# Kernel tuning notes

Hardware: AMD Instinct MI355X
Metric: run time of the kernel (lower is better)

## Reference

```python
import jax, jax.numpy as jnp
import numpy as np

N_ENT = 100000
N_REL = 200
D_IN = 128
D_HID = 128
D_OUT = 128
N_BASES = 50
N_EDGES = 800000
N_TRIPLES = 4096
BN_EPS = 1e-5


def setup_inputs() -> dict:
    key = jax.random.key(0)
    ks = jax.random.split(key, 16)
    xavier = lambda k, shape: jax.random.normal(k, shape, jnp.float32) * np.sqrt(2.0 / (shape[-2] + shape[-1]))
    inp = {
        'entity_embeds': xavier(ks[0], (N_ENT, D_IN)),
        'bases': xavier(ks[1], (N_BASES, D_IN)),
        'coefficients': xavier(ks[2], (N_REL, N_BASES)),
        'self_rel_embed': xavier(ks[3], (1, D_IN)),
        'W1': xavier(ks[4], (3, D_IN, D_HID)),
        'relw1': xavier(ks[5], (D_IN, D_HID)),
        'bn1_gamma': jnp.ones((D_HID,), jnp.float32),
        'bn1_beta': jnp.zeros((D_HID,), jnp.float32),
        'W2': xavier(ks[6], (3, D_HID, D_OUT)),
        'relw2': xavier(ks[7], (D_HID, D_OUT)),
        'bn2_gamma': jnp.ones((D_OUT,), jnp.float32),
        'bn2_beta': jnp.zeros((D_OUT,), jnp.float32),
        'ent_ids': jnp.arange(N_ENT, dtype=jnp.int32),
        'edge_index': jax.random.randint(ks[8], (2, N_EDGES), 0, N_ENT, jnp.int32),
        'edge_type': jax.random.randint(ks[9], (N_EDGES,), 0, 2 * N_REL + 1, jnp.int32),
        'y': jax.random.randint(ks[10], (N_EDGES,), 0, 3, jnp.int32),
    }
    heads = jax.random.randint(ks[11], (N_TRIPLES,), 0, N_ENT, jnp.int32)
    rels = jax.random.randint(ks[12], (N_TRIPLES,), 0, 2 * N_REL + 1, jnp.int32)
    tails = jax.random.randint(ks[13], (N_TRIPLES,), 0, N_ENT, jnp.int32)
    inp['triples'] = jnp.stack([heads, rels, tails], axis=1)
    return inp


def _compgcn_layer(x, r, edge_index, edge_type, y, W, relw, gamma, beta):
    src, dst = edge_index[0], edge_index[1]
    # message: gather neighbor & relation embeds, edge-direction-conditioned matmul
    msgs = x[src] - r[edge_type]                      # [E, d_in]
    out = jnp.zeros((msgs.shape[0], W.shape[-1]), msgs.dtype)
    for k in range(3):  # y in {0,1,2}: masked matmul instead of [E,d,d] gather
        mask = (y == k)[:, None]
        out = out + jnp.where(mask, msgs, 0.0) @ W[k]
    # scatter-add aggregation at destination nodes
    agg = jax.ops.segment_sum(out, dst, num_segments=x.shape[0])  # [N, d_out]
    # BatchNorm1d (training-mode batch statistics, biased var)
    mean = jnp.mean(agg, axis=0)
    var = jnp.mean(jnp.square(agg - mean), axis=0)
    bn = (agg - mean) * jax.lax.rsqrt(var + BN_EPS) * gamma + beta
    return jnp.tanh(bn), r @ relw


def reference(entity_embeds, bases, coefficients, self_rel_embed, W1, relw1,
              bn1_gamma, bn1_beta, W2, relw2, bn2_gamma, bn2_beta,
              ent_ids, edge_index, edge_type, y, triples):
    x = entity_embeds[ent_ids]
    r = coefficients @ bases                           # basis-composed relations
    r = jnp.concatenate([r, -r, self_rel_embed], axis=0)  # [2R+1, d]
    x, r = _compgcn_layer(x, r, edge_index, edge_type, y, W1, relw1, bn1_gamma, bn1_beta)
    x, r = _compgcn_layer(x, r, edge_index, edge_type, y, W2, relw2, bn2_gamma, bn2_beta)
    # decode: TransE-style L1 score
    h = x[triples[:, 0]]
    re = r[triples[:, 1]]
    t = x[triples[:, 2]]
    scores = jnp.sum(jnp.abs(h + re - t), axis=1)      # p=1 norm
    return scores
```

## Files before the change

kernel.cpp:

```cpp
#include <hip/hip_runtime.h>
#include <cstdint>

typedef __attribute__((ext_vector_type(8))) short short8;
typedef __attribute__((ext_vector_type(4))) float f32x4;

static __device__ __forceinline__ unsigned short f2bf(float f) {
  unsigned int u = __float_as_uint(f);
  unsigned int r = (u + 0x7FFFu + ((u >> 16) & 1u)) >> 16;
  return (unsigned short)r;
}
static __device__ __forceinline__ unsigned int pack2bf(float a, float b) {
  return (unsigned int)f2bf(a) | ((unsigned int)f2bf(b) << 16);
}
static __device__ __forceinline__ float2 bf2f(unsigned int u) {
  return make_float2(__uint_as_float(u << 16), __uint_as_float(u & 0xFFFF0000u));
}
static __device__ __forceinline__ void acc8(float* a, uint4 h, uint4 r) {
  float2 f, g;
  f = bf2f(h.x); g = bf2f(r.x); a[0] += f.x - g.x; a[1] += f.y - g.y;
  f = bf2f(h.y); g = bf2f(r.y); a[2] += f.x - g.x; a[3] += f.y - g.y;
  f = bf2f(h.z); g = bf2f(r.z); a[4] += f.x - g.x; a[5] += f.y - g.y;
  f = bf2f(h.w); g = bf2f(r.w); a[6] += f.x - g.x; a[7] += f.y - g.y;
}

__global__ void k_rfull(const float* __restrict__ coeff, const float* __restrict__ bases,
                        const float* __restrict__ selfr, float* __restrict__ rfull,
                        unsigned int* __restrict__ rfb) {
  __shared__ float row_s[128];
  int row = blockIdx.x, c = threadIdx.x;
  float v;
  if (row == 400) {
    v = selfr[c];
  } else {
    int rr = row < 200 ? row : row - 200;
    float s = 0.f;
#pragma unroll 10
    for (int b = 0; b < 50; ++b) s += coeff[rr * 50 + b] * bases[b * 128 + c];
    v = (row < 200) ? s : -s;
  }
  rfull[row * 128 + c] = v;
  row_s[c] = v;
  __syncthreads();
  if (c < 64) rfb[row * 64 + c] = pack2bf(row_s[2 * c], row_s[2 * c + 1]);
}

__global__ void k_rmm(const float* __restrict__ A, const float* __restrict__ B,
                      float* __restrict__ out, unsigned int* __restrict__ outb) {
  __shared__ float row_s[128];
  int r = blockIdx.x, c = threadIdx.x;
  float s = 0.f;
#pragma unroll 8
  for (int k = 0; k < 128; ++k) s += A[r * 128 + k] * B[k * 128 + c];
  out[r * 128 + c] = s;
  if (outb) {
    row_s[c] = s;
    __syncthreads();
    if (c < 64) outb[r * 64 + c] = pack2bf(row_s[2 * c], row_s[2 * c + 1]);
  }
}

__global__ void k_cvt(const float* __restrict__ src, unsigned int* __restrict__ dst, int nPairs) {
  int i = blockIdx.x * blockDim.x + threadIdx.x;
  if (i >= nPairs) return;
  float2 v = *(const float2*)&src[(size_t)i * 2];
  dst[i] = pack2bf(v.x, v.y);
}

__global__ void k_wconv2(const float* __restrict__ W1, const float* __restrict__ W2,
                         unsigned short* __restrict__ WT1, unsigned short* __restrict__ WT2) {
  int gid = blockIdx.x * 256 + threadIdx.x;
  const int half = 128 * 384;
  const float* W = (gid < half) ? W1 : W2;
  unsigned short* WT = (gid < half) ? WT1 : WT2;
  int idx = (gid < half) ? gid : gid - half;
  int n = idx & 127, k = idx >> 7;
  int kk = k >> 7, kr = k & 127;
  WT[(size_t)n * 384 + k] = f2bf(W[(size_t)kk * 16384 + kr * 128 + n]);
}

__global__ __launch_bounds__(256) void k_histR(const int* __restrict__ ei, const int* __restrict__ y,
                                               int* __restrict__ counts, int nE, int rsz) {
  int r = blockIdx.x;
  int e0 = blockIdx.y * 1024;
#pragma unroll
  for (int i = 0; i < 4; ++i) {
    int e = e0 + i * 256 + threadIdx.x;
    if (e < nE) {
      int key = ei[nE + e] * 3 + y[e];
      if (key / rsz == r) atomicAdd(&counts[key], 1);
    }
  }
}

__global__ void k_scan1(const int* __restrict__ counts, int* __restrict__ local,
                        int* __restrict__ blockSums, int n) {
  __shared__ int sdata[1024];
  int tid = threadIdx.x;
  int i = blockIdx.x * 1024 + tid;
  int v = (i < n) ? counts[i] : 0;
  sdata[tid] = v;
  __syncthreads();
  for (int off = 1; off < 1024; off <<= 1) {
    int t = (tid >= off) ? sdata[tid - off] : 0;
    __syncthreads();
    sdata[tid] += t;
    __syncthreads();
  }
  if (i < n) local[i] = sdata[tid] - v;
  if (tid == 1023) blockSums[blockIdx.x] = sdata[1023];
}

__global__ void k_scan2(const int* __restrict__ blockSums, int* __restrict__ carries,
                        int* __restrict__ offsets, int n, int nb) {
  __shared__ int sdata[1024];
  int tid = threadIdx.x;
  int v = (tid < nb) ? blockSums[tid] : 0;
  sdata[tid] = v;
  __syncthreads();
  for (int off = 1; off < 1024; off <<= 1) {
    int t = (tid >= off) ? sdata[tid - off] : 0;
    __syncthreads();
    sdata[tid] += t;
    __syncthreads();
  }
  if (tid < nb) carries[tid] = sdata[tid] - v;
  if (tid == 1023) offsets[n] = sdata[1023];
}

__global__ void k_scan3(const int* __restrict__ local, const int* __restrict__ carries,
                        int* __restrict__ offsets, int* __restrict__ cursor, int n) {
  int i = blockIdx.x * 1024 + threadIdx.x;
  if (i >= n) return;
  int v = local[i] + carries[blockIdx.x];
  offsets[i] = v;
  cursor[i] = v;
}

__global__ __launch_bounds__(256) void k_fillR(const int* __restrict__ ei, const int* __restrict__ et,
                                               const int* __restrict__ y, int* __restrict__ cursor,
                                               unsigned int* __restrict__ bucket, int nE, int rsz) {
  int r = blockIdx.x;
  int e0 = blockIdx.y * 1024;
#pragma unroll
  for (int i = 0; i < 4; ++i) {
    int e = e0 + i * 256 + threadIdx.x;
    if (e < nE) {
      int key = ei[nE + e] * 3 + y[e];
      if (key / rsz == r) {
        int slot = atomicAdd(&cursor[key], 1);
        bucket[slot] = (unsigned int)ei[e] | ((unsigned int)et[e] << 20);
      }
    }
  }
}

__global__ __launch_bounds__(256) void k_agg4(const unsigned int* __restrict__ xb,
                                              const int* __restrict__ ids,
                                              const unsigned int* __restrict__ rb,
                                              const int* __restrict__ offsets,
                                              const unsigned int* __restrict__ packed,
                                              unsigned short* __restrict__ T,
                                              float* __restrict__ statZero, int nKeys) {
  if (blockIdx.x == 0) statZero[threadIdx.x] = 0.f;
  int wid = blockIdx.x * 4 + (threadIdx.x >> 6);
  int lane = threadIdx.x & 63;
  int quad = lane >> 4, l16 = lane & 15;
  int key = wid * 4 + quad;
  if (key >= nKeys) return;
  int dst = key / 3, k = key - dst * 3;
  int s = offsets[key], e = offsets[key + 1];
  float a0[8] = {}, a1[8] = {};
  int j = s;
  for (; j + 1 < e; j += 2) {
    unsigned int p0 = packed[j], p1 = packed[j + 1];
    int s0 = p0 & 0xFFFFF, t0 = p0 >> 20;
    int s1 = p1 & 0xFFFFF, t1 = p1 >> 20;
    if (ids) { s0 = ids[s0]; s1 = ids[s1]; }
    uint4 h0 = *(const uint4*)&xb[(size_t)s0 * 64 + l16 * 4];
    uint4 r0 = *(const uint4*)&rb[(size_t)t0 * 64 + l16 * 4];
    uint4 h1 = *(const uint4*)&xb[(size_t)s1 * 64 + l16 * 4];
    uint4 r1 = *(const uint4*)&rb[(size_t)t1 * 64 + l16 * 4];
    acc8(a0, h0, r0);
    acc8(a1, h1, r1);
  }
  if (j < e) {
    unsigned int p0 = packed[j];
    int s0 = p0 & 0xFFFFF, t0 = p0 >> 20;
    if (ids) s0 = ids[s0];
    uint4 h0 = *(const uint4*)&xb[(size_t)s0 * 64 + l16 * 4];
    uint4 r0 = *(const uint4*)&rb[(size_t)t0 * 64 + l16 * 4];
    acc8(a0, h0, r0);
  }
  uint4 o;
  o.x = pack2bf(a0[0] + a1[0], a0[1] + a1[1]);
  o.y = pack2bf(a0[2] + a1[2], a0[3] + a1[3]);
  o.z = pack2bf(a0[4] + a1[4], a0[5] + a1[5]);
  o.w = pack2bf(a0[6] + a1[6], a0[7] + a1[7]);
  *(uint4*)&T[(size_t)dst * 384 + k * 128 + l16 * 8] = o;
}

__global__ __launch_bounds__(256) void k_gemm_mfma(const unsigned short* __restrict__ A,
                                                   const unsigned short* __restrict__ WT,
                                                   unsigned short* __restrict__ C,
                                                   float* __restrict__ sums,
                                                   float* __restrict__ sumsq, int M) {
  __shared__ unsigned short As[2][128][40];
  __shared__ unsigned short Bs[2][128][40];
  __shared__ float sSum[128], sSq[128];
  const int tid = threadIdx.x;
  const int m0 = blockIdx.x * 128;
  const int wave = tid >> 6, lane = tid & 63;
  const int wrow = wave >> 1, wcol = wave & 1;
  const int quad = lane >> 4, l16 = lane & 15;
  f32x4 acc[4][4] = {};

  const int rr0 = tid >> 2, kc0 = (tid & 3) * 8;
  const int rr1 = rr0 + 64;
  const int ma0 = m0 + rr0, ma1 = m0 + rr1;
  const float4 fz = make_float4(0.f, 0.f, 0.f, 0.f);

  float4 apf0, apf1, bpf0, bpf1;
  apf0 = (ma0 < M) ? *(const float4*)&A[(size_t)ma0 * 384 + kc0] : fz;
  apf1 = (ma1 < M) ? *(const float4*)&A[(size_t)ma1 * 384 + kc0] : fz;
  bpf0 = *(const float4*)&WT[(size_t)rr0 * 384 + kc0];
  bpf1 = *(const float4*)&WT[(size_t)rr1 * 384 + kc0];
  *(float4*)&As[0][rr0][kc0] = apf0;
  *(float4*)&As[0][rr1][kc0] = apf1;
  *(float4*)&Bs[0][rr0][kc0] = bpf0;
  *(float4*)&Bs[0][rr1][kc0] = bpf1;
  __syncthreads();

  for (int it = 0; it < 12; ++it) {
    const int cur = it & 1;
    const int nxt = cur ^ 1;
    const bool pf = (it < 11);
    if (pf) {
      int kb = (it + 1) * 32;
      apf0 = (ma0 < M) ? *(const float4*)&A[(size_t)ma0 * 384 + kb + kc0] : fz;
      apf1 = (ma1 < M) ? *(const float4*)&A[(size_t)ma1 * 384 + kb + kc0] : fz;
      bpf0 = *(const float4*)&WT[(size_t)rr0 * 384 + kb + kc0];
      bpf1 = *(const float4*)&WT[(size_t)rr1 * 384 + kb + kc0];
    }
    short8 a[4], b[4];
#pragma unroll
    for (int t = 0; t < 4; ++t) a[t] = *(const short8*)&As[cur][wrow * 64 + t * 16 + l16][quad * 8];
#pragma unroll
    for (int t = 0; t < 4; ++t) b[t] = *(const short8*)&Bs[cur][wcol * 64 + t * 16 + l16][quad * 8];
#pragma unroll
    for (int rt = 0; rt < 4; ++rt)
#pragma unroll
      for (int ct = 0; ct < 4; ++ct)
        acc[rt][ct] = __builtin_amdgcn_mfma_f32_16x16x32_bf16(a[rt], b[ct], acc[rt][ct], 0, 0, 0);
    if (pf) {
      *(float4*)&As[nxt][rr0][kc0] = apf0;
      *(float4*)&As[nxt][rr1][kc0] = apf1;
      *(float4*)&Bs[nxt][rr0][kc0] = bpf0;
      *(float4*)&Bs[nxt][rr1][kc0] = bpf1;
      __syncthreads();
    }
  }

  if (tid < 128) { sSum[tid] = 0.f; sSq[tid] = 0.f; }
  __syncthreads();
  float ps[4] = {}, pq[4] = {};
#pragma unroll
  for (int rt = 0; rt < 4; ++rt) {
#pragma unroll
    for (int reg = 0; reg < 4; ++reg) {
      int m = m0 + wrow * 64 + rt * 16 + quad * 4 + reg;
      if (m < M) {
#pragma unroll
        for (int ct = 0; ct < 4; ++ct) {
          float v = acc[rt][ct][reg];
          int col = wcol * 64 + ct * 16 + l16;
          C[(size_t)m * 128 + col] = f2bf(v);
          ps[ct] += v; pq[ct] += v * v;
        }
      }
    }
  }
#pragma unroll
  for (int ct = 0; ct < 4; ++ct) {
    int col = wcol * 64 + ct * 16 + l16;
    atomicAdd(&sSum[col], ps[ct]);
    atomicAdd(&sSq[col], pq[ct]);
  }
  __syncthreads();
  if (tid < 128) {
    atomicAdd(&sums[tid], sSum[tid]);
    atomicAdd(&sumsq[tid], sSq[tid]);
  }
}

__global__ void k_norm(const unsigned int* __restrict__ Cb,
                       const float* __restrict__ sums, const float* __restrict__ sumsq,
                       const float* __restrict__ gamma, const float* __restrict__ beta,
                       float invN, unsigned int* __restrict__ xb, int nPairs) {
  __shared__ float sc_s[128], bi_s[128];
  if (threadIdx.x < 128) {
    int c = threadIdx.x;
    float mean = sums[c] * invN;
    float var = fmaxf(sumsq[c] * invN - mean * mean, 0.f);
    float sc = rsqrtf(var + 1e-5f) * gamma[c];
    sc_s[c] = sc;
    bi_s[c] = beta[c] - mean * sc;
  }
  __syncthreads();
  int i = blockIdx.x * blockDim.x + threadIdx.x;
  if (i >= nPairs) return;
  int j = i & 63;
  float2 v = bf2f(Cb[i]);
  float a = tanhf(fmaf(v.x, sc_s[2 * j], bi_s[2 * j]));
  float b = tanhf(fmaf(v.y, sc_s[2 * j + 1], bi_s[2 * j + 1]));
  xb[i] = pack2bf(a, b);
}

__global__ void k_score(const unsigned int* __restrict__ xb, const float* __restrict__ r,
                        const int* __restrict__ triples, float* __restrict__ out, int nT) {
  int gid = blockIdx.x * blockDim.x + threadIdx.x;
  int t = gid >> 6;
  if (t >= nT) return;
  int lane = gid & 63;
  int h = triples[t * 3], rel = triples[t * 3 + 1], tl = triples[t * 3 + 2];
  float2 a = bf2f(xb[(size_t)h * 64 + lane]);
  float2 b = *(const float2*)&r[(size_t)rel * 128 + lane * 2];
  float2 cc = bf2f(xb[(size_t)tl * 64 + lane]);
  float s = fabsf(a.x + b.x - cc.x) + fabsf(a.y + b.y - cc.y);
#pragma unroll
  for (int off = 32; off > 0; off >>= 1) s += __shfl_down(s, off);
  if (lane == 0) out[t] = s;
}

extern "C" void kernel_launch(void* const* d_in, const int* in_sizes, int n_in,
                              void* d_out, int out_size, void* d_ws, size_t ws_size,
                              hipStream_t stream) {
  const float* ent   = (const float*)d_in[0];
  const float* bases = (const float*)d_in[1];
  const float* coeff = (const float*)d_in[2];
  const float* selfr = (const float*)d_in[3];
  const float* W1    = (const float*)d_in[4];
  const float* relw1 = (const float*)d_in[5];
  const float* g1    = (const float*)d_in[6];
  const float* b1    = (const float*)d_in[7];
  const float* W2    = (const float*)d_in[8];
  const float* relw2 = (const float*)d_in[9];
  const float* g2    = (const float*)d_in[10];
  const float* b2    = (const float*)d_in[11];
  const int* ent_ids = (const int*)d_in[12];
  const int* ei      = (const int*)d_in[13];
  const int* et      = (const int*)d_in[14];
  const int* yk      = (const int*)d_in[15];
  const int* triples = (const int*)d_in[16];

  const int M  = in_sizes[0] / 128;
  const int nE = in_sizes[14];
  const int nT = in_sizes[16] / 3;
  const int nKeys = M * 3;
  const int nScanBlocks = (nKeys + 1023) / 1024;
  const int rsz = (nKeys + 7) / 8;

  float* p = (float*)d_ws;
  float* rfull = p; p += 401 * 128;
  float* r1    = p; p += 401 * 128;
  float* r2    = p; p += 401 * 128;
  float* sums  = p; p += 128;
  float* sumsq = p; p += 128;
  unsigned short* Cb  = (unsigned short*)p;
  unsigned int* entbf = (unsigned int*)Cb;
  unsigned int* xb    = (unsigned int*)(Cb + (size_t)M * 128);
  unsigned int* rfb   = xb + (size_t)M * 64;
  unsigned int* r1b   = rfb + 401 * 64;
  unsigned short* T   = (unsigned short*)(r1b + 401 * 64);
  unsigned short* WT1 = T + (size_t)M * 384;
  unsigned short* WT2 = WT1 + 128 * 384;
  int* counts  = (int*)(WT2 + 128 * 384);
  int* offsets = counts + nKeys;
  int* cursor  = offsets + nKeys + 1;
  int* slocal  = cursor + nKeys;
  int* sblock  = slocal + nKeys;
  int* scarry  = sblock + nScanBlocks;
  unsigned int* bucket = (unsigned int*)(scarry + nScanBlocks);

  float* out = (float*)d_out;

  const int mfmaBlocks = (M + 127) / 128;
  const int nPairs = M * 64;
  const int pairBlocks = (nPairs + 255) / 256;
  const int aggBlocks  = (nKeys + 15) / 16;
  const dim3 rangedGrid(8, (nE + 1023) / 1024);

  k_rfull<<<401, 128, 0, stream>>>(coeff, bases, selfr, rfull, rfb);
  k_rmm<<<401, 128, 0, stream>>>(rfull, relw1, r1, r1b);
  k_rmm<<<401, 128, 0, stream>>>(r1, relw2, r2, nullptr);
  k_cvt<<<pairBlocks, 256, 0, stream>>>(ent, entbf, nPairs);
  k_wconv2<<<384, 256, 0, stream>>>(W1, W2, WT1, WT2);

  hipMemsetAsync(counts, 0, (size_t)nKeys * sizeof(int), stream);
  k_histR<<<rangedGrid, 256, 0, stream>>>(ei, yk, counts, nE, rsz);
  k_scan1<<<nScanBlocks, 1024, 0, stream>>>(counts, slocal, sblock, nKeys);
  k_scan2<<<1, 1024, 0, stream>>>(sblock, scarry, offsets, nKeys, nScanBlocks);
  k_scan3<<<nScanBlocks, 1024, 0, stream>>>(slocal, scarry, offsets, cursor, nKeys);
  k_fillR<<<rangedGrid, 256, 0, stream>>>(ei, et, yk, cursor, bucket, nE, rsz);

  k_agg4<<<aggBlocks, 256, 0, stream>>>(entbf, ent_ids, rfb, offsets, bucket, T, sums, nKeys);
  k_gemm_mfma<<<mfmaBlocks, 256, 0, stream>>>(T, WT1, Cb, sums, sumsq, M);
  k_norm<<<pairBlocks, 256, 0, stream>>>((unsigned int*)Cb, sums, sumsq, g1, b1, 1.0f / M, xb, nPairs);

  k_agg4<<<aggBlocks, 256, 0, stream>>>(xb, nullptr, r1b, offsets, bucket, T, sums, nKeys);
  k_gemm_mfma<<<mfmaBlocks, 256, 0, stream>>>(T, WT2, Cb, sums, sumsq, M);
  k_norm<<<pairBlocks, 256, 0, stream>>>((unsigned int*)Cb, sums, sumsq, g2, b2, 1.0f / M, xb, nPairs);

  k_score<<<(nT * 64 + 255) / 256, 256, 0, stream>>>(xb, r2, triples, out, nT);
}
```

Before: 462.5 us.

## Fuse edge aggregation into MFMA GEMM and merge prep kernels

The per-destination gather-aggregation now writes its bf16 rows directly into shared memory, and the MFMA GEMM with batch-norm statistics runs in the same kernel. This removes the round-trip of the large intermediate T matrix through global memory and two launches per layer. Relation composition, the two relation matmuls, weight transposition, entity conversion with the ent_ids gather, and zeroing of counters and stats are merged into one multi-role prep kernel, and the norm kernel is vectorised to uint4. In exchange, the fused kernel uses about 50KB of shared memory with 64-row tiles, which may limit occupancy, and it streams B operands from global memory without staging them in shared memory.

```diff
diff --git a/kernel.cpp b/kernel.cpp
--- a/kernel.cpp
+++ b/kernel.cpp
@@ -23,59 +23,77 @@
   f = bf2f(h.w); g = bf2f(r.w); a[6] += f.x - g.x; a[7] += f.y - g.y;
 }
 
-__global__ void k_rfull(const float* __restrict__ coeff, const float* __restrict__ bases,
-                        const float* __restrict__ selfr, float* __restrict__ rfull,
-                        unsigned int* __restrict__ rfb) {
-  __shared__ float row_s[128];
-  int row = blockIdx.x, c = threadIdx.x;
-  float v;
-  if (row == 400) {
-    v = selfr[c];
+__global__ __launch_bounds__(256) void k_prep(
+    const float* __restrict__ coeff, const float* __restrict__ bases,
+    const float* __restrict__ selfr, const float* __restrict__ relw1,
+    const float* __restrict__ relw2,
+    unsigned int* __restrict__ rfb, unsigned int* __restrict__ r1b,
+    float* __restrict__ r2,
+    const float* __restrict__ W1, const float* __restrict__ W2,
+    unsigned short* __restrict__ WT1, unsigned short* __restrict__ WT2,
+    const float* __restrict__ ent, const int* __restrict__ ent_ids,
+    unsigned int* __restrict__ entbf,
+    int* __restrict__ counts, float* __restrict__ stats,
+    int nPairs, int nKeys, int cvtB, int cntB) {
+  int b = blockIdx.x, tid = threadIdx.x;
+  if (b < 201) {
+    __shared__ float row[2][128], r1row[2][128];
+    int half = tid >> 7, c = tid & 127;
+    int r = 2 * b + half;
+    bool ok = (r <= 400);
+    if (ok) {
+      float v;
+      if (r == 400) {
+        v = selfr[c];
+      } else {
+        int rr = (r < 200) ? r : r - 200;
+        float s = 0.f;
+#pragma unroll 10
+        for (int k = 0; k < 50; ++k) s += coeff[rr * 50 + k] * bases[k * 128 + c];
+        v = (r < 200) ? s : -s;
+      }
+      row[half][c] = v;
+    }
+    __syncthreads();
+    if (ok && c < 64) rfb[r * 64 + c] = pack2bf(row[half][2 * c], row[half][2 * c + 1]);
+    if (ok) {
+      float s = 0.f;
+#pragma unroll 8
+      for (int k = 0; k < 128; ++k) s += row[half][k] * relw1[k * 128 + c];
+      r1row[half][c] = s;
+    }
+    __syncthreads();
+    if (ok && c < 64) r1b[r * 64 + c] = pack2bf(r1row[half][2 * c], r1row[half][2 * c + 1]);
+    if (ok) {
+      float s = 0.f;
+#pragma unroll 8
+      for (int k = 0; k < 128; ++k) s += r1row[half][k] * relw2[k * 128 + c];
+      r2[r * 128 + c] = s;
+    }
+  } else if (b < 585) {
+    int idx = (b - 201) * 256 + tid;
+    const int half = 128 * 384;
+    const float* W = (idx < half) ? W1 : W2;
+    unsigned short* WT = (idx < half) ? WT1 : WT2;
+    int id2 = (idx < half) ? idx : idx - half;
+    int n = id2 & 127, k = id2 >> 7;
+    int kk = k >> 7, kr = k & 127;
+    WT[(size_t)n * 384 + k] = f2bf(W[(size_t)kk * 16384 + kr * 128 + n]);
+  } else if (b < 585 + cvtB) {
+    int i = (b - 585) * 256 + tid;
+    if (i < nPairs) {
+      int e = i >> 6;
+      int src = ent_ids[e];
+      float2 v = *(const float2*)&ent[(size_t)src * 128 + (i & 63) * 2];
+      entbf[i] = pack2bf(v.x, v.y);
+    }
+  } else if (b < 585 + cvtB + cntB) {
+    int i = (b - (585 + cvtB)) * 256 + tid;
+    if (i < nKeys) counts[i] = 0;
   } else {
-    int rr = row < 200 ? row : row - 200;
-    float s = 0.f;
-#pragma unroll 10
-    for (int b = 0; b < 50; ++b) s += coeff[rr * 50 + b] * bases[b * 128 + c];
-    v = (row < 200) ? s : -s;
-  }
-  rfull[row * 128 + c] = v;
-  row_s[c] = v;
-  __syncthreads();
-  if (c < 64) rfb[row * 64 + c] = pack2bf(row_s[2 * c], row_s[2 * c + 1]);
-}
-
-__global__ void k_rmm(const float* __restrict__ A, const float* __restrict__ B,
-                      float* __restrict__ out, unsigned int* __restrict__ outb) {
-  __shared__ float row_s[128];
-  int r = blockIdx.x, c = threadIdx.x;
-  float s = 0.f;
-#pragma unroll 8
-  for (int k = 0; k < 128; ++k) s += A[r * 128 + k] * B[k * 128 + c];
-  out[r * 128 + c] = s;
-  if (outb) {
-    row_s[c] = s;
-    __syncthreads();
-    if (c < 64) outb[r * 64 + c] = pack2bf(row_s[2 * c], row_s[2 * c + 1]);
-  }
-}
-
-__global__ void k_cvt(const float* __restrict__ src, unsigned int* __restrict__ dst, int nPairs) {
-  int i = blockIdx.x * blockDim.x + threadIdx.x;
-  if (i >= nPairs) return;
-  float2 v = *(const float2*)&src[(size_t)i * 2];
-  dst[i] = pack2bf(v.x, v.y);
-}
-
-__global__ void k_wconv2(const float* __restrict__ W1, const float* __restrict__ W2,
-                         unsigned short* __restrict__ WT1, unsigned short* __restrict__ WT2) {
-  int gid = blockIdx.x * 256 + threadIdx.x;
-  const int half = 128 * 384;
-  const float* W = (gid < half) ? W1 : W2;
-  unsigned short* WT = (gid < half) ? WT1 : WT2;
-  int idx = (gid < half) ? gid : gid - half;
-  int n = idx & 127, k = idx >> 7;
-  int kk = k >> 7, kr = k & 127;
-  WT[(size_t)n * 384 + k] = f2bf(W[(size_t)kk * 16384 + kr * 128 + n]);
+    stats[tid] = 0.f;
+    stats[tid + 256] = 0.f;
+  }
 }
 
 __global__ __launch_bounds__(256) void k_histR(const int* __restrict__ ei, const int* __restrict__ y,
@@ -154,125 +172,91 @@
   }
 }
 
-__global__ __launch_bounds__(256) void k_agg4(const unsigned int* __restrict__ xb,
-                                              const int* __restrict__ ids,
-                                              const unsigned int* __restrict__ rb,
-                                              const int* __restrict__ offsets,
-                                              const unsigned int* __restrict__ packed,
-                                              unsigned short* __restrict__ T,
-                                              float* __restrict__ statZero, int nKeys) {
-  if (blockIdx.x == 0) statZero[threadIdx.x] = 0.f;
-  int wid = blockIdx.x * 4 + (threadIdx.x >> 6);
-  int lane = threadIdx.x & 63;
-  int quad = lane >> 4, l16 = lane & 15;
-  int key = wid * 4 + quad;
-  if (key >= nKeys) return;
-  int dst = key / 3, k = key - dst * 3;
-  int s = offsets[key], e = offsets[key + 1];
-  float a0[8] = {}, a1[8] = {};
-  int j = s;
-  for (; j + 1 < e; j += 2) {
-    unsigned int p0 = packed[j], p1 = packed[j + 1];
-    int s0 = p0 & 0xFFFFF, t0 = p0 >> 20;
-    int s1 = p1 & 0xFFFFF, t1 = p1 >> 20;
-    if (ids) { s0 = ids[s0]; s1 = ids[s1]; }
-    uint4 h0 = *(const uint4*)&xb[(size_t)s0 * 64 + l16 * 4];
-    uint4 r0 = *(const uint4*)&rb[(size_t)t0 * 64 + l16 * 4];
-    uint4 h1 = *(const uint4*)&xb[(size_t)s1 * 64 + l16 * 4];
-    uint4 r1 = *(const uint4*)&rb[(size_t)t1 * 64 + l16 * 4];
-    acc8(a0, h0, r0);
-    acc8(a1, h1, r1);
-  }
-  if (j < e) {
-    unsigned int p0 = packed[j];
-    int s0 = p0 & 0xFFFFF, t0 = p0 >> 20;
-    if (ids) s0 = ids[s0];
-    uint4 h0 = *(const uint4*)&xb[(size_t)s0 * 64 + l16 * 4];
-    uint4 r0 = *(const uint4*)&rb[(size_t)t0 * 64 + l16 * 4];
-    acc8(a0, h0, r0);
-  }
-  uint4 o;
-  o.x = pack2bf(a0[0] + a1[0], a0[1] + a1[1]);
-  o.y = pack2bf(a0[2] + a1[2], a0[3] + a1[3]);
-  o.z = pack2bf(a0[4] + a1[4], a0[5] + a1[5]);
-  o.w = pack2bf(a0[6] + a1[6], a0[7] + a1[7]);
-  *(uint4*)&T[(size_t)dst * 384 + k * 128 + l16 * 8] = o;
-}
-
-__global__ __launch_bounds__(256) void k_gemm_mfma(const unsigned short* __restrict__ A,
-                                                   const unsigned short* __restrict__ WT,
-                                                   unsigned short* __restrict__ C,
-                                                   float* __restrict__ sums,
-                                                   float* __restrict__ sumsq, int M) {
-  __shared__ unsigned short As[2][128][40];
-  __shared__ unsigned short Bs[2][128][40];
+__global__ __launch_bounds__(256, 3) void k_fused(
+    const unsigned int* __restrict__ xb, const unsigned int* __restrict__ rb,
+    const int* __restrict__ offsets, const unsigned int* __restrict__ packed,
+    const unsigned short* __restrict__ WT, unsigned short* __restrict__ C,
+    float* __restrict__ sums, float* __restrict__ sumsq, int M) {
+  __shared__ unsigned short As[64][392];
   __shared__ float sSum[128], sSq[128];
   const int tid = threadIdx.x;
-  const int m0 = blockIdx.x * 128;
+  const int m0 = blockIdx.x * 64;
   const int wave = tid >> 6, lane = tid & 63;
-  const int wrow = wave >> 1, wcol = wave & 1;
   const int quad = lane >> 4, l16 = lane & 15;
-  f32x4 acc[4][4] = {};
-
-  const int rr0 = tid >> 2, kc0 = (tid & 3) * 8;
-  const int rr1 = rr0 + 64;
-  const int ma0 = m0 + rr0, ma1 = m0 + rr1;
-  const float4 fz = make_float4(0.f, 0.f, 0.f, 0.f);
-
-  float4 apf0, apf1, bpf0, bpf1;
-  apf0 = (ma0 < M) ? *(const float4*)&A[(size_t)ma0 * 384 + kc0] : fz;
-  apf1 = (ma1 < M) ? *(const float4*)&A[(size_t)ma1 * 384 + kc0] : fz;
-  bpf0 = *(const float4*)&WT[(size_t)rr0 * 384 + kc0];
-  bpf1 = *(const float4*)&WT[(size_t)rr1 * 384 + kc0];
-  *(float4*)&As[0][rr0][kc0] = apf0;
-  *(float4*)&As[0][rr1][kc0] = apf1;
-  *(float4*)&Bs[0][rr0][kc0] = bpf0;
-  *(float4*)&Bs[0][rr1][kc0] = bpf1;
+  const int qid = (wave << 2) | quad;
+  if (tid < 128) { sSum[tid] = 0.f; sSq[tid] = 0.f; }
+
+#pragma unroll 1
+  for (int i = 0; i < 12; ++i) {
+    int kloc = qid * 12 + i;
+    int dloc = kloc / 3, cls = kloc - dloc * 3;
+    float a0[8] = {}, a1[8] = {};
+    int dst = m0 + dloc;
+    if (dst < M) {
+      int key = dst * 3 + cls;
+      int s = offsets[key], e = offsets[key + 1];
+      int j = s;
+      for (; j + 1 < e; j += 2) {
+        unsigned int p0 = packed[j], p1 = packed[j + 1];
+        int s0 = p0 & 0xFFFFF, t0 = p0 >> 20;
+        int s1 = p1 & 0xFFFFF, t1 = p1 >> 20;
+        uint4 h0 = *(const uint4*)&xb[(size_t)s0 * 64 + l16 * 4];
+        uint4 r0 = *(const uint4*)&rb[(size_t)t0 * 64 + l16 * 4];
+        uint4 h1 = *(const uint4*)&xb[(size_t)s1 * 64 + l16 * 4];
+        uint4 r1 = *(const uint4*)&rb[(size_t)t1 * 64 + l16 * 4];
+        acc8(a0, h0, r0);
+        acc8(a1, h1, r1);
+      }
+      if (j < e) {
+        unsigned int p0 = packed[j];
+        int s0 = p0 & 0xFFFFF, t0 = p0 >> 20;
+        uint4 h0 = *(const uint4*)&xb[(size_t)s0 * 64 + l16 * 4];
+        uint4 r0 = *(const uint4*)&rb[(size_t)t0 * 64 + l16 * 4];
+        acc8(a0, h0, r0);
+      }
+    }
+    uint4 o;
+    o.x = pack2bf(a0[0] + a1[0], a0[1] + a1[1]);
+    o.y = pack2bf(a0[2] + a1[2], a0[3] + a1[3]);
+    o.z = pack2bf(a0[4] + a1[4], a0[5] + a1[5]);
+    o.w = pack2bf(a0[6] + a1[6], a0[7] + a1[7]);
+    *(uint4*)&As[dloc][cls * 128 + l16 * 8] = o;
+  }
   __syncthreads();
 
+  const unsigned short* Wp = WT + (size_t)(wave * 32 + l16) * 384 + quad * 8;
+  short8 bc0 = *(const short8*)(Wp);
+  short8 bc1 = *(const short8*)(Wp + 16 * 384);
+  f32x4 acc[4][2] = {};
+#pragma unroll 1
   for (int it = 0; it < 12; ++it) {
-    const int cur = it & 1;
-    const int nxt = cur ^ 1;
-    const bool pf = (it < 11);
-    if (pf) {
-      int kb = (it + 1) * 32;
-      apf0 = (ma0 < M) ? *(const float4*)&A[(size_t)ma0 * 384 + kb + kc0] : fz;
-      apf1 = (ma1 < M) ? *(const float4*)&A[(size_t)ma1 * 384 + kb + kc0] : fz;
-      bpf0 = *(const float4*)&WT[(size_t)rr0 * 384 + kb + kc0];
-      bpf1 = *(const float4*)&WT[(size_t)rr1 * 384 + kb + kc0];
-    }
-    short8 a[4], b[4];
-#pragma unroll
-    for (int t = 0; t < 4; ++t) a[t] = *(const short8*)&As[cur][wrow * 64 + t * 16 + l16][quad * 8];
-#pragma unroll
-    for (int t = 0; t < 4; ++t) b[t] = *(const short8*)&Bs[cur][wcol * 64 + t * 16 + l16][quad * 8];
-#pragma unroll
-    for (int rt = 0; rt < 4; ++rt)
-#pragma unroll
-      for (int ct = 0; ct < 4; ++ct)
-        acc[rt][ct] = __builtin_amdgcn_mfma_f32_16x16x32_bf16(a[rt], b[ct], acc[rt][ct], 0, 0, 0);
-    if (pf) {
-      *(float4*)&As[nxt][rr0][kc0] = apf0;
-      *(float4*)&As[nxt][rr1][kc0] = apf1;
-      *(float4*)&Bs[nxt][rr0][kc0] = bpf0;
-      *(float4*)&Bs[nxt][rr1][kc0] = bpf1;
-      __syncthreads();
-    }
-  }
-
-  if (tid < 128) { sSum[tid] = 0.f; sSq[tid] = 0.f; }
-  __syncthreads();
-  float ps[4] = {}, pq[4] = {};
-#pragma unroll
-  for (int rt = 0; rt < 4; ++rt) {
+    short8 bn0, bn1;
+    if (it < 11) {
+      bn0 = *(const short8*)(Wp + (it + 1) * 32);
+      bn1 = *(const short8*)(Wp + 16 * 384 + (it + 1) * 32);
+    }
+    short8 a[4];
+#pragma unroll
+    for (int t = 0; t < 4; ++t) a[t] = *(const short8*)&As[t * 16 + l16][it * 32 + quad * 8];
+#pragma unroll
+    for (int t = 0; t < 4; ++t) {
+      acc[t][0] = __builtin_amdgcn_mfma_f32_16x16x32_bf16(a[t], bc0, acc[t][0], 0, 0, 0);
+      acc[t][1] = __builtin_amdgcn_mfma_f32_16x16x32_bf16(a[t], bc1, acc[t][1], 0, 0, 0);
+    }
+    if (it < 11) { bc0 = bn0; bc1 = bn1; }
+  }
+
+  float ps[2] = {}, pq[2] = {};
+#pragma unroll
+  for (int t = 0; t < 4; ++t) {
 #pragma unroll
     for (int reg = 0; reg < 4; ++reg) {
-      int m = m0 + wrow * 64 + rt * 16 + quad * 4 + reg;
+      int m = m0 + t * 16 + quad * 4 + reg;
       if (m < M) {
 #pragma unroll
-        for (int ct = 0; ct < 4; ++ct) {
-          float v = acc[rt][ct][reg];
-          int col = wcol * 64 + ct * 16 + l16;
+        for (int ct = 0; ct < 2; ++ct) {
+          float v = acc[t][ct][reg];
+          int col = wave * 32 + ct * 16 + l16;
           C[(size_t)m * 128 + col] = f2bf(v);
           ps[ct] += v; pq[ct] += v * v;
         }
@@ -280,8 +264,8 @@
     }
   }
 #pragma unroll
-  for (int ct = 0; ct < 4; ++ct) {
-    int col = wcol * 64 + ct * 16 + l16;
+  for (int ct = 0; ct < 2; ++ct) {
+    int col = wave * 32 + ct * 16 + l16;
     atomicAdd(&sSum[col], ps[ct]);
     atomicAdd(&sSq[col], pq[ct]);
   }
@@ -292,10 +276,10 @@
   }
 }
 
-__global__ void k_norm(const unsigned int* __restrict__ Cb,
+__global__ void k_norm(const uint4* __restrict__ Cb4,
                        const float* __restrict__ sums, const float* __restrict__ sumsq,
                        const float* __restrict__ gamma, const float* __restrict__ beta,
-                       float invN, unsigned int* __restrict__ xb, int nPairs) {
+                       float invN, uint4* __restrict__ xb4, int nQuad) {
   __shared__ float sc_s[128], bi_s[128];
   if (threadIdx.x < 128) {
     int c = threadIdx.x;
@@ -307,12 +291,20 @@
   }
   __syncthreads();
   int i = blockIdx.x * blockDim.x + threadIdx.x;
-  if (i >= nPairs) return;
-  int j = i & 63;
-  float2 v = bf2f(Cb[i]);
-  float a = tanhf(fmaf(v.x, sc_s[2 * j], bi_s[2 * j]));
-  float b = tanhf(fmaf(v.y, sc_s[2 * j + 1], bi_s[2 * j + 1]));
-  xb[i] = pack2bf(a, b);
+  if (i >= nQuad) return;
+  uint4 v = Cb4[i];
+  int j = (i * 4) & 63;
+  uint4 o;
+  float2 f;
+  f = bf2f(v.x);
+  o.x = pack2bf(tanhf(fmaf(f.x, sc_s[2*j],   bi_s[2*j])),   tanhf(fmaf(f.y, sc_s[2*j+1], bi_s[2*j+1])));
+  f = bf2f(v.y);
+  o.y = pack2bf(tanhf(fmaf(f.x, sc_s[2*j+2], bi_s[2*j+2])), tanhf(fmaf(f.y, sc_s[2*j+3], bi_s[2*j+3])));
+  f = bf2f(v.z);
+  o.z = pack2bf(tanhf(fmaf(f.x, sc_s[2*j+4], bi_s[2*j+4])), tanhf(fmaf(f.y, sc_s[2*j+5], bi_s[2*j+5])));
+  f = bf2f(v.w);
+  o.w = pack2bf(tanhf(fmaf(f.x, sc_s[2*j+6], bi_s[2*j+6])), tanhf(fmaf(f.y, sc_s[2*j+7], bi_s[2*j+7])));
+  xb4[i] = o;
 }
 
 __global__ void k_score(const unsigned int* __restrict__ xb, const float* __restrict__ r,
@@ -360,18 +352,14 @@
   const int rsz = (nKeys + 7) / 8;
 
   float* p = (float*)d_ws;
-  float* rfull = p; p += 401 * 128;
-  float* r1    = p; p += 401 * 128;
   float* r2    = p; p += 401 * 128;
-  float* sums  = p; p += 128;
-  float* sumsq = p; p += 128;
+  float* stats = p; p += 512;
   unsigned short* Cb  = (unsigned short*)p;
-  unsigned int* entbf = (unsigned int*)Cb;
-  unsigned int* xb    = (unsigned int*)(Cb + (size_t)M * 128);
+  unsigned int* entbf = (unsigned int*)(Cb + (size_t)M * 128);
+  unsigned int* xb    = entbf + (size_t)M * 64;
   unsigned int* rfb   = xb + (size_t)M * 64;
   unsigned int* r1b   = rfb + 401 * 64;
-  unsigned short* T   = (unsigned short*)(r1b + 401 * 64);
-  unsigned short* WT1 = T + (size_t)M * 384;
+  unsigned short* WT1 = (unsigned short*)(r1b + 401 * 64);
   unsigned short* WT2 = WT1 + 128 * 384;
   int* counts  = (int*)(WT2 + 128 * 384);
   int* offsets = counts + nKeys;
@@ -381,34 +369,39 @@
   int* scarry  = sblock + nScanBlocks;
   unsigned int* bucket = (unsigned int*)(scarry + nScanBlocks);
 
+  float* sums1 = stats, *sumsq1 = stats + 128;
+  float* sums2 = stats + 256, *sumsq2 = stats + 384;
   float* out = (float*)d_out;
 
-  const int mfmaBlocks = (M + 127) / 128;
   const int nPairs = M * 64;
-  const int pairBlocks = (nPairs + 255) / 256;
-  const int aggBlocks  = (nKeys + 15) / 16;
+  const int nQuad  = M * 16;
+  const int cvtB = (nPairs + 255) / 256;
+  const int cntB = (nKeys + 255) / 256;
+  const int prepBlocks = 585 + cvtB + cntB + 1;
+  const int fusedBlocks = (M + 63) / 64;
+  const int normBlocks = (nQuad + 255) / 256;
   const dim3 rangedGrid(8, (nE + 1023) / 1024);
 
-  k_rfull<<<401, 128, 0, stream>>>(coeff, bases, selfr, rfull, rfb);
-  k_rmm<<<401, 128, 0, stream>>>(rfull, relw1, r1, r1b);
-  k_rmm<<<401, 128, 0, stream>>>(r1, relw2, r2, nullptr);
-  k_cvt<<<pairBlocks, 256, 0, stream>>>(ent, entbf, nPairs);
-  k_wconv2<<<384, 256, 0, stream>>>(W1, W2, WT1, WT2);
-
-  hipMemsetAsync(counts, 0, (size_t)nKeys * sizeof(int), stream);
+  k_prep<<<prepBlocks, 256, 0, stream>>>(coeff, bases, selfr, relw1, relw2,
+                                         rfb, r1b, r2, W1, W2, WT1, WT2,
+                                         ent, ent_ids, entbf, counts, stats,
+                                         nPairs, nKeys, cvtB, cntB);
+
   k_histR<<<rangedGrid, 256, 0, stream>>>(ei, yk, counts, nE, rsz);
   k_scan1<<<nScanBlocks, 1024, 0, stream>>>(counts, slocal, sblock, nKeys);
   k_scan2<<<1, 1024, 0, stream>>>(sblock, scarry, offsets, nKeys, nScanBlocks);
   k_scan3<<<nScanBlocks, 1024, 0, stream>>>(slocal, scarry, offsets, cursor, nKeys);
   k_fillR<<<rangedGrid, 256, 0, stream>>>(ei, et, yk, cursor, bucket, nE, rsz);
 
-  k_agg4<<<aggBlocks, 256, 0, stream>>>(entbf, ent_ids, rfb, offsets, bucket, T, sums, nKeys);
-  k_gemm_mfma<<<mfmaBlocks, 256, 0, stream>>>(T, WT1, Cb, sums, sumsq, M);
-  k_norm<<<pairBlocks, 256, 0, stream>>>((unsigned int*)Cb, sums, sumsq, g1, b1, 1.0f / M, xb, nPairs);
-
-  k_agg4<<<aggBlocks, 256, 0, stream>>>(xb, nullptr, r1b, offsets, bucket, T, sums, nKeys);
-  k_gemm_mfma<<<mfmaBlocks, 256, 0, stream>>>(T, WT2, Cb, sums, sumsq, M);
-  k_norm<<<pairBlocks, 256, 0, stream>>>((unsigned int*)Cb, sums, sumsq, g2, b2, 1.0f / M, xb, nPairs);
+  k_fused<<<fusedBlocks, 256, 0, stream>>>(entbf, rfb, offsets, bucket, WT1,
+                                           Cb, sums1, sumsq1, M);
+  k_norm<<<normBlocks, 256, 0, stream>>>((const uint4*)Cb, sums1, sumsq1, g1, b1,
+                                         1.0f / M, (uint4*)xb, nQuad);
+
+  k_fused<<<fusedBlocks, 256, 0, stream>>>(xb, r1b, offsets, bucket, WT2,
+                                           Cb, sums2, sumsq2, M);
+  k_norm<<<normBlocks, 256, 0, stream>>>((const uint4*)Cb, sums2, sumsq2, g2, b2,
+                                         1.0f / M, (uint4*)xb, nQuad);
 
   k_score<<<(nT * 64 + 255) / 256, 256, 0, stream>>>(xb, r2, triples, out, nT);
 }
```

Result: slower. 503.2 us (+8.8%).
